# Optimization experiments

Hardware: AMD Instinct MI355X
Metric: run time of the kernel (lower is better)

## Reference

```python
import jax, jax.numpy as jnp
import numpy as np

D_MODEL = 1024
N_HEADS = 16
HEAD_DIM = D_MODEL // N_HEADS


def setup_inputs() -> dict:
    key = jax.random.key(0)
    ks = jax.random.split(key, 5)
    B, T = 4, 2048
    scale = 0.02
    x = jax.random.normal(ks[0], (B, T, D_MODEL), dtype=jnp.float32)
    W_qkv = jax.random.normal(ks[1], (D_MODEL, 3 * D_MODEL), dtype=jnp.float32) * scale
    b_qkv = jnp.zeros((3 * D_MODEL,), dtype=jnp.float32)
    W_out = jax.random.normal(ks[2], (D_MODEL, D_MODEL), dtype=jnp.float32) * scale
    b_out = jnp.zeros((D_MODEL,), dtype=jnp.float32)
    return {"x": x, "W_qkv": W_qkv, "b_qkv": b_qkv, "W_out": W_out, "b_out": b_out}


def reference(x, W_qkv, b_qkv, W_out, b_out):
    B, T, C = x.shape
    H, Dh = N_HEADS, HEAD_DIM
    qkv = x @ W_qkv + b_qkv                      # (B,T,3C)
    q, k, v = jnp.split(qkv, 3, axis=-1)
    # (B,T,C) -> (B,H,T,Dh)
    q = q.reshape(B, T, H, Dh).transpose(0, 2, 1, 3)
    k = k.reshape(B, T, H, Dh).transpose(0, 2, 1, 3)
    v = v.reshape(B, T, H, Dh).transpose(0, 2, 1, 3)
    scores = jnp.einsum("bhqd,bhkd->bhqk", q, k) / jnp.sqrt(jnp.float32(Dh))
    causal = jnp.tril(jnp.ones((T, T), dtype=bool))  # True = keep
    scores = jnp.where(causal, scores, jnp.float32(-jnp.inf))
    attn = jax.nn.softmax(scores, axis=-1)
    out = jnp.einsum("bhqk,bhkd->bhqd", attn, v)  # (B,H,T,Dh)
    concat = out.transpose(0, 2, 1, 3).reshape(B, T, C)
    return concat @ W_out + b_out
```

## Files before the change

kernel.cpp:

```cpp
#include <hip/hip_runtime.h>
#include <math.h>

typedef __attribute__((ext_vector_type(8))) short bf16x8;
typedef __attribute__((ext_vector_type(4))) float f32x4;
typedef unsigned short u16;
typedef unsigned int u32;

#define TSEQ 2048
#define NH   16
#define DH   64
#define CDIM 1024
#define SCLQ 0.18033688011112042f

__device__ __forceinline__ u16 f2bf(float f) {
    union { float f; u32 u; } v; v.f = f;
    u32 r = v.u + 0x7fffu + ((v.u >> 16) & 1u);
    return (u16)(r >> 16);
}

__device__ __forceinline__ u32 cvtpk(float lo, float hi) {
    u32 r;
    asm("v_cvt_pk_bf16_f32 %0, %1, %2" : "=v"(r) : "v"(lo), "v"(hi));
    return r;
}

__device__ __forceinline__ float max3f(float a, float b, float c) {
    return fmaxf(fmaxf(a, b), c);
}

__device__ __forceinline__ void gl_lds16(const void* g, void* l) {
    __builtin_amdgcn_global_load_lds(
        (const __attribute__((address_space(1))) u32*)g,
        (__attribute__((address_space(3))) u32*)l, 16, 0, 0);
}

#define MFMA16(a, b, c) __builtin_amdgcn_mfma_f32_16x16x32_bf16(a, b, c, 0, 0, 0)

__global__ __launch_bounds__(256) void cvt_bf16(const float* __restrict__ in,
                                                u16* __restrict__ out, int n) {
    int i = (blockIdx.x * 256 + threadIdx.x) * 8;
    if (i >= n) return;
    float4 a = *(const float4*)(in + i);
    float4 b = *(const float4*)(in + i + 4);
    u16 o[8] = {f2bf(a.x), f2bf(a.y), f2bf(a.z), f2bf(a.w),
                f2bf(b.x), f2bf(b.y), f2bf(b.z), f2bf(b.w)};
    *(uint4*)(out + i) = *(const uint4*)o;
}

__global__ __launch_bounds__(256) void tr_w_bf16(const float* __restrict__ Wf,
                                                 u16* __restrict__ Wt, int K, int N) {
    __shared__ float tile[32][33];
    int n0 = blockIdx.x * 32, k0 = blockIdx.y * 32;
    int tx = threadIdx.x, ty = threadIdx.y;
#pragma unroll
    for (int r = 0; r < 4; r++)
        tile[ty + r * 8][tx] = Wf[(k0 + ty + r * 8) * N + n0 + tx];
    __syncthreads();
#pragma unroll
    for (int r = 0; r < 4; r++)
        Wt[(n0 + ty + r * 8) * K + k0 + tx] = f2bf(tile[tx][ty + r * 8]);
}

__global__ __launch_bounds__(256) void qkv_gemm_bf(
    const u16* __restrict__ A, const u16* __restrict__ Bt,
    const float* __restrict__ bias,
    u16* __restrict__ Qo, u16* __restrict__ Ko, u16* __restrict__ Vo) {
    __shared__ u16 Al[128 * 32];
    __shared__ u16 Bl[128 * 32];
    const int tid = threadIdx.x;
    const int lane = tid & 63, w = tid >> 6;
    const int l15 = lane & 15, l4 = lane >> 4;
    const int wm = w >> 1, wn = w & 1;
    const int mb = blockIdx.y * 128, nb = blockIdx.x * 128;
    const int KD = 1024;

    f32x4 zero = {0.f, 0.f, 0.f, 0.f};
    f32x4 acc[4][4];
#pragma unroll
    for (int i = 0; i < 4; i++)
#pragma unroll
        for (int j = 0; j < 4; j++) acc[i][j] = zero;

    for (int kb = 0; kb < KD; kb += 32) {
        __syncthreads();
#pragma unroll
        for (int r = 0; r < 2; r++) {
            int idx = r * 256 + tid;
            int row = idx >> 2, h = idx & 3;
            gl_lds16(A + (mb + row) * KD + kb + h * 8, Al + idx * 8);
            gl_lds16(Bt + (nb + row) * KD + kb + h * 8, Bl + idx * 8);
        }
        __syncthreads();
        bf16x8 af[4], bfr[4];
#pragma unroll
        for (int u = 0; u < 4; u++) {
            af[u]  = *(const bf16x8*)(Al + (wm * 64 + u * 16 + l15) * 32 + l4 * 8);
            bfr[u] = *(const bf16x8*)(Bl + (wn * 64 + u * 16 + l15) * 32 + l4 * 8);
        }
#pragma unroll
        for (int am = 0; am < 4; am++)
#pragma unroll
            for (int bn = 0; bn < 4; bn++)
                acc[am][bn] = MFMA16(af[am], bfr[bn], acc[am][bn]);
    }

#pragma unroll
    for (int am = 0; am < 4; am++)
#pragma unroll
        for (int bn = 0; bn < 4; bn++) {
            int n = nb + wn * 64 + bn * 16 + l15;
            int which = n >> 10, hh = (n >> 6) & 15, d = n & 63;
            float bz = bias[n];
            int m0 = mb + wm * 64 + am * 16 + l4 * 4;
            int b = m0 >> 11, t0 = m0 & 2047;
            if (which == 0) {
#pragma unroll
                for (int i = 0; i < 4; i++)
                    Qo[((b * NH + hh) * TSEQ + t0 + i) * DH + d] =
                        f2bf((acc[am][bn][i] + bz) * SCLQ);
            } else if (which == 1) {
#pragma unroll
                for (int i = 0; i < 4; i++)
                    Ko[((b * NH + hh) * TSEQ + t0 + i) * DH + d] =
                        f2bf(acc[am][bn][i] + bz);
            } else {
                u16 ov[4];
#pragma unroll
                for (int i = 0; i < 4; i++) ov[i] = f2bf(acc[am][bn][i] + bz);
                *(uint2*)&Vo[((b * NH + hh) * DH + d) * TSEQ + t0] =
                    *(const uint2*)ov;
            }
        }
}

__global__ __launch_bounds__(256) void out_gemm_bf(
    const u16* __restrict__ A, const u16* __restrict__ Bt,
    const float* __restrict__ bias, float* __restrict__ Out) {
    __shared__ u16 Al[128 * 32];
    __shared__ u16 Bl[128 * 32];
    const int tid = threadIdx.x;
    const int lane = tid & 63, w = tid >> 6;
    const int l15 = lane & 15, l4 = lane >> 4;
    const int wm = w >> 1, wn = w & 1;
    const int mb = blockIdx.y * 128, nb = blockIdx.x * 128;
    const int KD = 1024;

    f32x4 zero = {0.f, 0.f, 0.f, 0.f};
    f32x4 acc[4][4];
#pragma unroll
    for (int i = 0; i < 4; i++)
#pragma unroll
        for (int j = 0; j < 4; j++) acc[i][j] = zero;

    for (int kb = 0; kb < KD; kb += 32) {
        __syncthreads();
#pragma unroll
        for (int r = 0; r < 2; r++) {
            int idx = r * 256 + tid;
            int row = idx >> 2, h = idx & 3;
            gl_lds16(A + (mb + row) * KD + kb + h * 8, Al + idx * 8);
            gl_lds16(Bt + (nb + row) * KD + kb + h * 8, Bl + idx * 8);
        }
        __syncthreads();
        bf16x8 af[4], bfr[4];
#pragma unroll
        for (int u = 0; u < 4; u++) {
            af[u]  = *(const bf16x8*)(Al + (wm * 64 + u * 16 + l15) * 32 + l4 * 8);
            bfr[u] = *(const bf16x8*)(Bl + (wn * 64 + u * 16 + l15) * 32 + l4 * 8);
        }
#pragma unroll
        for (int am = 0; am < 4; am++)
#pragma unroll
            for (int bn = 0; bn < 4; bn++)
                acc[am][bn] = MFMA16(af[am], bfr[bn], acc[am][bn]);
    }

#pragma unroll
    for (int am = 0; am < 4; am++)
#pragma unroll
        for (int bn = 0; bn < 4; bn++) {
            int n = nb + wn * 64 + bn * 16 + l15;
            float bz = bias[n];
#pragma unroll
            for (int i = 0; i < 4; i++) {
                int m = mb + wm * 64 + am * 16 + l4 * 4 + i;
                Out[m * CDIM + n] = acc[am][bn][i] + bz;
            }
        }
}

__global__ __launch_bounds__(256, 4) void attn_mfma(
    const u16* __restrict__ Q, const u16* __restrict__ K,
    const u16* __restrict__ Vt, u16* __restrict__ Oc) {
    __shared__ u16 Kl[2][4096];
    __shared__ u16 Vl[2][4096];
    __shared__ u16 Pl[4096];

    const int tid = threadIdx.x;
    const int lane = tid & 63, w = tid >> 6;
    const int l15 = lane & 15, l4 = lane >> 4;
    const int bh = blockIdx.x & 63;
    const int pair = blockIdx.x >> 6;
    const int qt0 = pair, qt1 = 31 - pair;
    const int NT = qt1 + 1;

    const u16* Qb = Q + bh * TSEQ * DH;
    const u16* Kb = K + bh * TSEQ * DH;
    const u16* Vb = Vt + bh * DH * TSEQ;

    auto STAGE = [&](int kt, int p) {
#pragma unroll
        for (int r = 0; r < 2; r++) {
            int idx = r * 256 + tid;
            int row = idx >> 3, h = idx & 7;
            int hs = h ^ (row & 7);
            gl_lds16(Kb + (kt * 64 + row) * DH + hs * 8, &Kl[p][idx * 8]);
            gl_lds16(Vb + row * TSEQ + kt * 64 + hs * 8, &Vl[p][idx * 8]);
        }
    };

    const int qrow0 = qt0 * 64 + w * 16 + l15;
    const int qrow1 = qt1 * 64 + w * 16 + l15;
    bf16x8 q0a, q0b, q1a, q1b;
    {
        const u16* qp = Qb + qrow0 * DH + l4 * 8;
        q0a = *(const bf16x8*)(qp);
        q0b = *(const bf16x8*)(qp + 32);
    }
    {
        const u16* qp = Qb + qrow1 * DH + l4 * 8;
        q1a = *(const bf16x8*)(qp);
        q1b = *(const bf16x8*)(qp + 32);
    }

    f32x4 zero = {0.f, 0.f, 0.f, 0.f};
    f32x4 o0[4], o1[4];
    float m0 = -INFINITY, l0 = 0.f, m1 = -INFINITY, l1 = 0.f;
#pragma unroll
    for (int i = 0; i < 4; i++) { o0[i] = zero; o1[i] = zero; }

    auto SMPV = [&](f32x4* s, float& m_r, float& l_r, f32x4* oacc,
                    int q_row, bool domask, int kt, int p) {
        if (domask) {
#pragma unroll
            for (int c = 0; c < 4; c++)
#pragma unroll
                for (int i = 0; i < 4; i++) {
                    int kg = kt * 64 + c * 16 + l4 * 4 + i;
                    if (kg > q_row) s[c][i] = -INFINITY;
                }
        }
        float a0 = max3f(s[0][0], s[0][1], s[0][2]);
        float a1 = max3f(s[0][3], s[1][0], s[1][1]);
        float a2 = max3f(s[1][2], s[1][3], s[2][0]);
        float a3 = max3f(s[2][1], s[2][2], s[2][3]);
        float a4 = max3f(s[3][0], s[3][1], s[3][2]);
        float mx = max3f(max3f(a0, a1, a2), fmaxf(a3, a4), s[3][3]);
        mx = fmaxf(mx, __shfl_xor(mx, 16));
        mx = fmaxf(mx, __shfl_xor(mx, 32));
        if (!__all(mx <= m_r)) {
            float mnew = fmaxf(m_r, mx);
            float corr = __builtin_amdgcn_exp2f(m_r - mnew);
            l_r *= corr;
            float cr[4];
#pragma unroll
            for (int r = 0; r < 4; r++) cr[r] = __shfl(corr, l4 * 4 + r);
#pragma unroll
            for (int dg = 0; dg < 4; dg++)
#pragma unroll
                for (int r = 0; r < 4; r++) oacc[dg][r] *= cr[r];
            m_r = mnew;
        }
        float pv[16];
#pragma unroll
        for (int c = 0; c < 4; c++)
#pragma unroll
            for (int i = 0; i < 4; i++)
                pv[c * 4 + i] = __builtin_amdgcn_exp2f(s[c][i] - m_r);
        float t0 = (pv[0] + pv[1]) + (pv[2] + pv[3]);
        float t1 = (pv[4] + pv[5]) + (pv[6] + pv[7]);
        float t2 = (pv[8] + pv[9]) + (pv[10] + pv[11]);
        float t3 = (pv[12] + pv[13]) + (pv[14] + pv[15]);
        float rs = (t0 + t1) + (t2 + t3);
        rs += __shfl_xor(rs, 16);
        rs += __shfl_xor(rs, 32);
        l_r += rs;

#pragma unroll
        for (int c = 0; c < 4; c++) {
            uint2 pr;
            pr.x = cvtpk(pv[c * 4 + 0], pv[c * 4 + 1]);
            pr.y = cvtpk(pv[c * 4 + 2], pv[c * 4 + 3]);
            int g = (c << 1) + (l4 >> 1);
            int gp = g ^ (l15 & 7);
            *(uint2*)&Pl[w * 1024 + l15 * 64 + gp * 8 + ((l4 & 1) << 2)] = pr;
        }

        __builtin_amdgcn_s_setprio(1);
#pragma unroll
        for (int kk = 0; kk < 2; kk++) {
            int grp = ((kk << 2) + l4) ^ (l15 & 7);
            bf16x8 pf = *(const bf16x8*)&Pl[w * 1024 + l15 * 64 + grp * 8];
#pragma unroll
            for (int dg = 0; dg < 4; dg++) {
                int drow = (dg << 4) + l15;
                bf16x8 vf = *(const bf16x8*)(&Vl[p][drow * 64 + grp * 8]);
                oacc[dg] = MFMA16(pf, vf, oacc[dg]);
            }
        }
        __builtin_amdgcn_s_setprio(0);
    };

    STAGE(0, 0);

    for (int kt = 0; kt < NT; kt++) {
        const int p = kt & 1;
        __syncthreads();
        if (kt + 1 < NT) {
            STAGE(kt + 1, p ^ 1);
            asm volatile("s_waitcnt vmcnt(4)" ::: "memory");
        } else {
            asm volatile("s_waitcnt vmcnt(0)" ::: "memory");
        }
        __syncthreads();

        const bool act0 = (kt <= qt0);

        f32x4 s1[4], s0[4];
        __builtin_amdgcn_s_setprio(1);
#pragma unroll
        for (int c = 0; c < 4; c++) {
            int trow = c * 16 + l15;
            int sw = l15 & 7;
            bf16x8 kf0 = *(const bf16x8*)(&Kl[p][trow * 64 + (l4 ^ sw) * 8]);
            bf16x8 kf1 = *(const bf16x8*)(&Kl[p][trow * 64 + ((4 + l4) ^ sw) * 8]);
            f32x4 a = zero;
            a = MFMA16(kf0, q1a, a);
            a = MFMA16(kf1, q1b, a);
            s1[c] = a;
            if (act0) {
                f32x4 b = zero;
                b = MFMA16(kf0, q0a, b);
                b = MFMA16(kf1, q0b, b);
                s0[c] = b;
            }
        }
        __builtin_amdgcn_s_setprio(0);

        SMPV(s1, m1, l1, o1, qrow1, kt == qt1, kt, p);
        if (act0) {
            asm volatile("s_waitcnt lgkmcnt(0)" ::: "memory");
            SMPV(s0, m0, l0, o0, qrow0, kt == qt0, kt, p);
        }
    }

    const int b = bh >> 4, hh = bh & 15;
    {
        float inv[4];
#pragma unroll
        for (int r = 0; r < 4; r++) inv[r] = 1.0f / __shfl(l0, l4 * 4 + r);
        int tb = qt0 * 64 + w * 16 + l4 * 4;
#pragma unroll
        for (int r = 0; r < 4; r++)
#pragma unroll
            for (int dg = 0; dg < 4; dg++)
                Oc[(b * TSEQ + tb + r) * CDIM + hh * DH + (dg << 4) + l15] =
                    f2bf(o0[dg][r] * inv[r]);
    }
    {
        float inv[4];
#pragma unroll
        for (int r = 0; r < 4; r++) inv[r] = 1.0f / __shfl(l1, l4 * 4 + r);
        int tb = qt1 * 64 + w * 16 + l4 * 4;
#pragma unroll
        for (int r = 0; r < 4; r++)
#pragma unroll
            for (int dg = 0; dg < 4; dg++)
                Oc[(b * TSEQ + tb + r) * CDIM + hh * DH + (dg << 4) + l15] =
                    f2bf(o1[dg][r] * inv[r]);
    }
}

extern "C" void kernel_launch(void* const* d_in, const int* in_sizes, int n_in,
                              void* d_out, int out_size, void* d_ws, size_t ws_size,
                              hipStream_t stream) {
    const float* x     = (const float*)d_in[0];
    const float* W_qkv = (const float*)d_in[1];
    const float* b_qkv = (const float*)d_in[2];
    const float* W_out = (const float*)d_in[3];
    const float* b_out = (const float*)d_in[4];
    float* out = (float*)d_out;

    u16* xb  = (u16*)d_ws;
    u16* Wqt = xb  + 8388608;
    u16* Wot = Wqt + 3145728;
    u16* Qw  = Wot + 1048576;
    u16* Kw  = Qw  + 8388608;
    u16* Vtw = Kw  + 8388608;
    u16* Ocw = Vtw + 8388608;

    cvt_bf16<<<4096, 256, 0, stream>>>(x, xb, 8388608);
    tr_w_bf16<<<dim3(96, 32), dim3(32, 8), 0, stream>>>(W_qkv, Wqt, 1024, 3072);
    tr_w_bf16<<<dim3(32, 32), dim3(32, 8), 0, stream>>>(W_out, Wot, 1024, 1024);
    qkv_gemm_bf<<<dim3(24, 64), 256, 0, stream>>>(xb, Wqt, b_qkv, Qw, Kw, Vtw);
    attn_mfma<<<1024, 256, 0, stream>>>(Qw, Kw, Vtw, Ocw);
    out_gemm_bf<<<dim3(8, 64), 256, 0, stream>>>(Ocw, Wot, b_out, out);
}
```

Baseline: 271.9 us.

## Replace GEMM kernels with 8-wave pipelined, swizzled 128x256 tile GEMM

Both the QKV and output projections now use one templated GEMM that runs 8 waves over a 128x256 tile with K-step 64. LDS is double-buffered and XOR-swizzled to avoid bank conflicts, and global-to-LDS loads are interleaved with MFMA phases using explicit barriers, waitcnts and setprio. Workgroups are remapped so that blocks sharing operands are grouped per XCD. The aim is to hide load latency and raise MFMA utilisation, at the cost of more LDS and a more fragile hand-written schedule.

Result: faster. 266.3 us (-2.1%).

```diff
diff --git a/kernel.cpp b/kernel.cpp
--- a/kernel.cpp
+++ b/kernel.cpp
@@ -35,6 +35,12 @@
 }
 
 #define MFMA16(a, b, c) __builtin_amdgcn_mfma_f32_16x16x32_bf16(a, b, c, 0, 0, 0)
+
+#define BAR()   do { __builtin_amdgcn_s_barrier(); __builtin_amdgcn_sched_barrier(0); } while (0)
+#define WAITV(n) do { asm volatile("s_waitcnt vmcnt(" #n ")" ::: "memory"); \
+                      __builtin_amdgcn_sched_barrier(0); } while (0)
+#define WAITL() do { asm volatile("s_waitcnt lgkmcnt(0)" ::: "memory"); \
+                     __builtin_amdgcn_sched_barrier(0); } while (0)
 
 __global__ __launch_bounds__(256) void cvt_bf16(const float* __restrict__ in,
                                                 u16* __restrict__ out, int n) {
@@ -61,18 +67,48 @@
         Wt[(n0 + ty + r * 8) * K + k0 + tx] = f2bf(tile[tx][ty + r * 8]);
 }
 
-__global__ __launch_bounds__(256) void qkv_gemm_bf(
+template <int EPI>
+__global__ __launch_bounds__(512, 2) void gemm_8p(
     const u16* __restrict__ A, const u16* __restrict__ Bt,
     const float* __restrict__ bias,
-    u16* __restrict__ Qo, u16* __restrict__ Ko, u16* __restrict__ Vo) {
-    __shared__ u16 Al[128 * 32];
-    __shared__ u16 Bl[128 * 32];
+    u16* __restrict__ O0, u16* __restrict__ O1, u16* __restrict__ O2,
+    float* __restrict__ Of) {
+    __shared__ u16 lA[2][128 * 64];
+    __shared__ u16 lB[2][2][128 * 64];
+
     const int tid = threadIdx.x;
     const int lane = tid & 63, w = tid >> 6;
     const int l15 = lane & 15, l4 = lane >> 4;
-    const int wm = w >> 1, wn = w & 1;
-    const int mb = blockIdx.y * 128, nb = blockIdx.x * 128;
+    const int wm = w >> 2, wn = w & 3;
+
+    const int nwg = gridDim.x, cpx = nwg >> 3;
+    const int wg = (blockIdx.x & 7) * cpx + (blockIdx.x >> 3);
+    const int mi = wg & 63, ni = wg >> 6;
+    const int mb = mi * 128, nb = ni * 256;
     const int KD = 1024;
+
+    auto stA = [&](int t, int p) {
+        int kb = (t & 15) * 64;
+#pragma unroll
+        for (int s = 0; s < 2; s++) {
+            int idx = s * 512 + tid;
+            int row = idx >> 3, g = idx & 7;
+            int gsw = g ^ (row & 7);
+            gl_lds16(A + (size_t)(mb + row) * KD + kb + gsw * 8, &lA[p][idx * 8]);
+        }
+    };
+    auto stB = [&](int t, int rb, int p) {
+        int kb = (t & 15) * 64;
+#pragma unroll
+        for (int s = 0; s < 2; s++) {
+            int idx = s * 512 + tid;
+            int row = idx >> 3, g = idx & 7;
+            int nrow = (row & 31) + ((row >> 5) << 6) + rb * 32;
+            int gsw = g ^ (row & 7);
+            gl_lds16(Bt + (size_t)(nb + nrow) * KD + kb + gsw * 8,
+                     &lB[p][rb][idx * 8]);
+        }
+    };
 
     f32x4 zero = {0.f, 0.f, 0.f, 0.f};
     f32x4 acc[4][4];
@@ -81,110 +117,140 @@
 #pragma unroll
         for (int j = 0; j < 4; j++) acc[i][j] = zero;
 
-    for (int kb = 0; kb < KD; kb += 32) {
-        __syncthreads();
-#pragma unroll
-        for (int r = 0; r < 2; r++) {
-            int idx = r * 256 + tid;
-            int row = idx >> 2, h = idx & 3;
-            gl_lds16(A + (mb + row) * KD + kb + h * 8, Al + idx * 8);
-            gl_lds16(Bt + (nb + row) * KD + kb + h * 8, Bl + idx * 8);
-        }
-        __syncthreads();
-        bf16x8 af[4], bfr[4];
-#pragma unroll
-        for (int u = 0; u < 4; u++) {
-            af[u]  = *(const bf16x8*)(Al + (wm * 64 + u * 16 + l15) * 32 + l4 * 8);
-            bfr[u] = *(const bf16x8*)(Bl + (wn * 64 + u * 16 + l15) * 32 + l4 * 8);
-        }
-#pragma unroll
-        for (int am = 0; am < 4; am++)
-#pragma unroll
-            for (int bn = 0; bn < 4; bn++)
-                acc[am][bn] = MFMA16(af[am], bfr[bn], acc[am][bn]);
-    }
-
-#pragma unroll
-    for (int am = 0; am < 4; am++)
-#pragma unroll
-        for (int bn = 0; bn < 4; bn++) {
-            int n = nb + wn * 64 + bn * 16 + l15;
-            int which = n >> 10, hh = (n >> 6) & 15, d = n & 63;
+    const int sw = l15 & 7;
+    const int aRow = wm * 64 + l15;
+    const int bRow = wn * 32 + l15;
+    const int g0 = (l4 ^ sw) * 8, g1 = ((4 + l4) ^ sw) * 8;
+
+    stA(0, 0); stB(0, 0, 0); stB(0, 1, 0);
+    stA(1, 1); stB(1, 0, 1);
+    WAITV(4);
+    BAR();
+
+    bf16x8 af[4][2], b0[2][2], b1[2][2];
+
+    for (int j = 0; j < 8; j++) {
+#pragma unroll
+        for (int fm = 0; fm < 4; fm++) {
+            const u16* base = &lA[0][(aRow + fm * 16) * 64];
+            af[fm][0] = *(const bf16x8*)(base + g0);
+            af[fm][1] = *(const bf16x8*)(base + g1);
+        }
+#pragma unroll
+        for (int fn = 0; fn < 2; fn++) {
+            const u16* base = &lB[0][0][(bRow + fn * 16) * 64];
+            b0[fn][0] = *(const bf16x8*)(base + g0);
+            b0[fn][1] = *(const bf16x8*)(base + g1);
+        }
+        stB(2 * j + 1, 1, 1);
+        BAR(); WAITL();
+        __builtin_amdgcn_s_setprio(1);
+#pragma unroll
+        for (int fm = 0; fm < 4; fm++)
+#pragma unroll
+            for (int fn = 0; fn < 2; fn++) {
+                acc[fm][fn] = MFMA16(af[fm][0], b0[fn][0], acc[fm][fn]);
+                acc[fm][fn] = MFMA16(af[fm][1], b0[fn][1], acc[fm][fn]);
+            }
+        __builtin_amdgcn_s_setprio(0);
+        BAR();
+#pragma unroll
+        for (int fn = 0; fn < 2; fn++) {
+            const u16* base = &lB[0][1][(bRow + fn * 16) * 64];
+            b1[fn][0] = *(const bf16x8*)(base + g0);
+            b1[fn][1] = *(const bf16x8*)(base + g1);
+        }
+        stA(2 * j + 2, 0); stB(2 * j + 2, 0, 0);
+        WAITV(4);
+        BAR(); WAITL();
+        __builtin_amdgcn_s_setprio(1);
+#pragma unroll
+        for (int fm = 0; fm < 4; fm++)
+#pragma unroll
+            for (int fn = 0; fn < 2; fn++) {
+                acc[fm][fn + 2] = MFMA16(af[fm][0], b1[fn][0], acc[fm][fn + 2]);
+                acc[fm][fn + 2] = MFMA16(af[fm][1], b1[fn][1], acc[fm][fn + 2]);
+            }
+        __builtin_amdgcn_s_setprio(0);
+        BAR();
+#pragma unroll
+        for (int fm = 0; fm < 4; fm++) {
+            const u16* base = &lA[1][(aRow + fm * 16) * 64];
+            af[fm][0] = *(const bf16x8*)(base + g0);
+            af[fm][1] = *(const bf16x8*)(base + g1);
+        }
+#pragma unroll
+        for (int fn = 0; fn < 2; fn++) {
+            const u16* base = &lB[1][0][(bRow + fn * 16) * 64];
+            b0[fn][0] = *(const bf16x8*)(base + g0);
+            b0[fn][1] = *(const bf16x8*)(base + g1);
+        }
+        stB(2 * j + 2, 1, 0);
+        BAR(); WAITL();
+        __builtin_amdgcn_s_setprio(1);
+#pragma unroll
+        for (int fm = 0; fm < 4; fm++)
+#pragma unroll
+            for (int fn = 0; fn < 2; fn++) {
+                acc[fm][fn] = MFMA16(af[fm][0], b0[fn][0], acc[fm][fn]);
+                acc[fm][fn] = MFMA16(af[fm][1], b0[fn][1], acc[fm][fn]);
+            }
+        __builtin_amdgcn_s_setprio(0);
+        BAR();
+#pragma unroll
+        for (int fn = 0; fn < 2; fn++) {
+            const u16* base = &lB[1][1][(bRow + fn * 16) * 64];
+            b1[fn][0] = *(const bf16x8*)(base + g0);
+            b1[fn][1] = *(const bf16x8*)(base + g1);
+        }
+        stA(2 * j + 3, 1); stB(2 * j + 3, 0, 1);
+        WAITV(4);
+        BAR(); WAITL();
+        __builtin_amdgcn_s_setprio(1);
+#pragma unroll
+        for (int fm = 0; fm < 4; fm++)
+#pragma unroll
+            for (int fn = 0; fn < 2; fn++) {
+                acc[fm][fn + 2] = MFMA16(af[fm][0], b1[fn][0], acc[fm][fn + 2]);
+                acc[fm][fn + 2] = MFMA16(af[fm][1], b1[fn][1], acc[fm][fn + 2]);
+            }
+        __builtin_amdgcn_s_setprio(0);
+        BAR();
+    }
+    asm volatile("s_waitcnt vmcnt(0)" ::: "memory");
+    __builtin_amdgcn_sched_barrier(0);
+
+#pragma unroll
+    for (int fm = 0; fm < 4; fm++)
+#pragma unroll
+        for (int fn = 0; fn < 4; fn++) {
+            int n = nb + wn * 64 + fn * 16 + l15;
+            int m0 = mb + wm * 64 + fm * 16 + l4 * 4;
             float bz = bias[n];
-            int m0 = mb + wm * 64 + am * 16 + l4 * 4;
-            int b = m0 >> 11, t0 = m0 & 2047;
-            if (which == 0) {
+            if (EPI == 0) {
 #pragma unroll
                 for (int i = 0; i < 4; i++)
-                    Qo[((b * NH + hh) * TSEQ + t0 + i) * DH + d] =
-                        f2bf((acc[am][bn][i] + bz) * SCLQ);
-            } else if (which == 1) {
-#pragma unroll
-                for (int i = 0; i < 4; i++)
-                    Ko[((b * NH + hh) * TSEQ + t0 + i) * DH + d] =
-                        f2bf(acc[am][bn][i] + bz);
+                    Of[(size_t)(m0 + i) * CDIM + n] = acc[fm][fn][i] + bz;
             } else {
-                u16 ov[4];
-#pragma unroll
-                for (int i = 0; i < 4; i++) ov[i] = f2bf(acc[am][bn][i] + bz);
-                *(uint2*)&Vo[((b * NH + hh) * DH + d) * TSEQ + t0] =
-                    *(const uint2*)ov;
-            }
-        }
-}
-
-__global__ __launch_bounds__(256) void out_gemm_bf(
-    const u16* __restrict__ A, const u16* __restrict__ Bt,
-    const float* __restrict__ bias, float* __restrict__ Out) {
-    __shared__ u16 Al[128 * 32];
-    __shared__ u16 Bl[128 * 32];
-    const int tid = threadIdx.x;
-    const int lane = tid & 63, w = tid >> 6;
-    const int l15 = lane & 15, l4 = lane >> 4;
-    const int wm = w >> 1, wn = w & 1;
-    const int mb = blockIdx.y * 128, nb = blockIdx.x * 128;
-    const int KD = 1024;
-
-    f32x4 zero = {0.f, 0.f, 0.f, 0.f};
-    f32x4 acc[4][4];
-#pragma unroll
-    for (int i = 0; i < 4; i++)
-#pragma unroll
-        for (int j = 0; j < 4; j++) acc[i][j] = zero;
-
-    for (int kb = 0; kb < KD; kb += 32) {
-        __syncthreads();
-#pragma unroll
-        for (int r = 0; r < 2; r++) {
-            int idx = r * 256 + tid;
-            int row = idx >> 2, h = idx & 3;
-            gl_lds16(A + (mb + row) * KD + kb + h * 8, Al + idx * 8);
-            gl_lds16(Bt + (nb + row) * KD + kb + h * 8, Bl + idx * 8);
-        }
-        __syncthreads();
-        bf16x8 af[4], bfr[4];
-#pragma unroll
-        for (int u = 0; u < 4; u++) {
-            af[u]  = *(const bf16x8*)(Al + (wm * 64 + u * 16 + l15) * 32 + l4 * 8);
-            bfr[u] = *(const bf16x8*)(Bl + (wn * 64 + u * 16 + l15) * 32 + l4 * 8);
-        }
-#pragma unroll
-        for (int am = 0; am < 4; am++)
-#pragma unroll
-            for (int bn = 0; bn < 4; bn++)
-                acc[am][bn] = MFMA16(af[am], bfr[bn], acc[am][bn]);
-    }
-
-#pragma unroll
-    for (int am = 0; am < 4; am++)
-#pragma unroll
-        for (int bn = 0; bn < 4; bn++) {
-            int n = nb + wn * 64 + bn * 16 + l15;
-            float bz = bias[n];
-#pragma unroll
-            for (int i = 0; i < 4; i++) {
-                int m = mb + wm * 64 + am * 16 + l4 * 4 + i;
-                Out[m * CDIM + n] = acc[am][bn][i] + bz;
+                int which = n >> 10, hh = (n >> 6) & 15, d = n & 63;
+                int b = m0 >> 11, t0 = m0 & 2047;
+                if (which == 0) {
+#pragma unroll
+                    for (int i = 0; i < 4; i++)
+                        O0[((b * NH + hh) * TSEQ + t0 + i) * DH + d] =
+                            f2bf((acc[fm][fn][i] + bz) * SCLQ);
+                } else if (which == 1) {
+#pragma unroll
+                    for (int i = 0; i < 4; i++)
+                        O1[((b * NH + hh) * TSEQ + t0 + i) * DH + d] =
+                            f2bf(acc[fm][fn][i] + bz);
+                } else {
+                    u16 ov[4];
+#pragma unroll
+                    for (int i = 0; i < 4; i++) ov[i] = f2bf(acc[fm][fn][i] + bz);
+                    *(uint2*)&O2[((b * NH + hh) * DH + d) * TSEQ + t0] =
+                        *(const uint2*)ov;
+                }
             }
         }
 }
@@ -331,9 +397,9 @@
 #pragma unroll
         for (int c = 0; c < 4; c++) {
             int trow = c * 16 + l15;
-            int sw = l15 & 7;
-            bf16x8 kf0 = *(const bf16x8*)(&Kl[p][trow * 64 + (l4 ^ sw) * 8]);
-            bf16x8 kf1 = *(const bf16x8*)(&Kl[p][trow * 64 + ((4 + l4) ^ sw) * 8]);
+            int swz = l15 & 7;
+            bf16x8 kf0 = *(const bf16x8*)(&Kl[p][trow * 64 + (l4 ^ swz) * 8]);
+            bf16x8 kf1 = *(const bf16x8*)(&Kl[p][trow * 64 + ((4 + l4) ^ swz) * 8]);
             f32x4 a = zero;
             a = MFMA16(kf0, q1a, a);
             a = MFMA16(kf1, q1b, a);
@@ -402,7 +468,7 @@
     cvt_bf16<<<4096, 256, 0, stream>>>(x, xb, 8388608);
     tr_w_bf16<<<dim3(96, 32), dim3(32, 8), 0, stream>>>(W_qkv, Wqt, 1024, 3072);
     tr_w_bf16<<<dim3(32, 32), dim3(32, 8), 0, stream>>>(W_out, Wot, 1024, 1024);
-    qkv_gemm_bf<<<dim3(24, 64), 256, 0, stream>>>(xb, Wqt, b_qkv, Qw, Kw, Vtw);
+    gemm_8p<1><<<768, 512, 0, stream>>>(xb, Wqt, b_qkv, Qw, Kw, Vtw, nullptr);
     attn_mfma<<<1024, 256, 0, stream>>>(Qw, Kw, Vtw, Ocw);
-    out_gemm_bf<<<dim3(8, 64), 256, 0, stream>>>(Ocw, Wot, b_out, out);
-}
+    gemm_8p<0><<<256, 512, 0, stream>>>(Ocw, Wot, b_out, nullptr, nullptr, nullptr, out);
+}
```
